# Kernel tuning notes

Measured on AMD Instinct MI355X. Metric: run time of the kernel, lower is better.

## Reference

```python
import jax, jax.numpy as jnp
import numpy as np

N = 50000      # nodes
E = 640000     # edges
FIN = 100      # raw node feature dim (nn.Linear(100, d_model))
D = 128        # d_model (dim_hidden)
H = 8          # num_heads
DH = D // H    # head dim
L = 4          # num_layers
DFF = 4 * D    # dim_feedforward
G = 64         # number of graphs in the batch
SCALE = DH ** -0.5


def setup_inputs() -> dict:
    key = jax.random.key(0)
    ks = jax.random.split(key, 12)
    x = jax.random.normal(ks[0], (N, FIN), jnp.float32)
    edge_index = jax.random.randint(ks[1], (2, E), 0, N, dtype=jnp.int64)
    batch = jnp.sort(jax.random.randint(ks[2], (N,), 0, G, dtype=jnp.int64))

    def w(k, shape, fan_in):
        return jax.random.normal(k, shape, jnp.float32) * (fan_in ** -0.5)

    W_embed = w(ks[3], (FIN, D), FIN)          # embedding, bias=False
    Wqk = w(ks[4], (L, D, 2 * D), D)           # to_qk, bias=False
    Wv = w(ks[5], (L, D, D), D)                # to_v, bias=False
    Wout = w(ks[6], (L, D, D), D)              # out_proj
    b_out = jnp.zeros((L, D), jnp.float32)
    W1 = w(ks[7], (L, D, DFF), D)              # FFN linear1
    b1 = jnp.zeros((L, DFF), jnp.float32)
    W2 = w(ks[8], (L, DFF, D), DFF)            # FFN linear2
    b2 = jnp.zeros((L, D), jnp.float32)
    return dict(x=x, edge_index=edge_index, batch=batch, W_embed=W_embed,
                Wqk=Wqk, Wv=Wv, Wout=Wout, b_out=b_out, W1=W1, b1=b1,
                W2=W2, b2=b2)


def reference(x, edge_index, batch, W_embed, Wqk, Wv, Wout, b_out, W1, b1, W2, b2):
    src = edge_index[0]  # j (message source)
    dst = edge_index[1]  # i (aggregation target)
    h = x @ W_embed  # [N, D]; dropout is identity at eval
    for l in range(L):
        # --- DAG multi-head attention (PyG MessagePassing, aggr='add') ---
        qk = h @ Wqk[l]
        q, k = qk[:, :D], qk[:, D:]
        v = h @ Wv[l]
        qj = q[src].reshape(E, H, DH)   # qk_j: gathered at source
        ki = k[dst].reshape(E, H, DH)   # qk_i: gathered at target
        logits = (qj * ki).sum(-1) * SCALE  # [E, H]
        # segment softmax over edges sharing the same target node
        m = jax.ops.segment_max(logits, dst, num_segments=N)        # [N, H]
        p = jnp.exp(logits - m[dst])
        ssum = jax.ops.segment_sum(p, dst, num_segments=N)          # [N, H]
        attn = p / ssum[dst]
        msg = (v[src].reshape(E, H, DH) * attn[:, :, None]).reshape(E, D)
        agg = jax.ops.segment_sum(msg, dst, num_segments=N)         # [N, D]
        h = h + (agg @ Wout[l] + b_out[l])   # residual; norm1 = Identity
        # --- FFN (relu) ---
        ff = jax.nn.relu(h @ W1[l] + b1[l]) @ W2[l] + b2[l]
        h = h + ff                            # residual; norm2 = Identity
    # global mean pool over graphs
    cnt = jax.ops.segment_sum(jnp.ones((N,), h.dtype), batch, num_segments=G)
    pooled = jax.ops.segment_sum(h, batch, num_segments=G) / jnp.maximum(cnt, 1.0)[:, None]
    return pooled
```

## Files before the change

kernel.cpp:

```cpp
#include <hip/hip_runtime.h>
#include <hip/hip_bf16.h>
#include <math.h>

#define D 128
#define NH 8
#define DFF 512
#define NG 64
#define NL 4
#define FIN 100
#define SCALE 0.25f
#define QKV 384

typedef __attribute__((ext_vector_type(8))) short short8;
typedef __attribute__((ext_vector_type(4))) float f32x4;

__device__ inline unsigned short f2bf(float v) {
    __hip_bfloat16 b = __float2bfloat16(v);
    return *reinterpret_cast<unsigned short*>(&b);
}

__global__ void count_kernel(const int* __restrict__ dst, int* __restrict__ cnt, int E) {
    int e = blockIdx.x * 256 + threadIdx.x;
    if (e < E) atomicAdd(&cnt[dst[e]], 1);
}

__global__ __launch_bounds__(1024) void scan_block_kernel(const int* __restrict__ cnt,
        int* __restrict__ incl, int* __restrict__ partials, int n) {
    __shared__ int s[1024];
    int tid = threadIdx.x;
    int gid = blockIdx.x * 1024 + tid;
    int val = (gid < n) ? cnt[gid] : 0;
    s[tid] = val;
    __syncthreads();
    for (int o = 1; o < 1024; o <<= 1) {
        int t = (tid >= o) ? s[tid - o] : 0;
        __syncthreads();
        s[tid] += t;
        __syncthreads();
    }
    if (gid < n) incl[gid] = s[tid];
    if (tid == 1023) partials[blockIdx.x] = s[1023];
}

__global__ void scan_partials_kernel(int* __restrict__ partials, int nb) {
    if (threadIdx.x == 0 && blockIdx.x == 0) {
        int run = 0;
        for (int i = 0; i < nb; ++i) { int t = partials[i]; partials[i] = run; run += t; }
    }
}

__global__ void finalize_off_kernel(const int* __restrict__ cnt, const int* __restrict__ incl,
        const int* __restrict__ partials, int* __restrict__ off, int* __restrict__ cur,
        int n, int E) {
    int gid = blockIdx.x * 256 + threadIdx.x;
    if (gid < n) {
        int v = incl[gid] - cnt[gid] + partials[gid >> 10];
        off[gid] = v;
        cur[gid] = v;
    }
    if (gid == 0) off[n] = E;
}

__global__ void scatter_kernel(const int* __restrict__ src, const int* __restrict__ dst,
        int* __restrict__ cur, int* __restrict__ csr_src, int E) {
    int e = blockIdx.x * 256 + threadIdx.x;
    if (e < E) {
        int p = atomicAdd(&cur[dst[e]], 1);
        csr_src[p] = src[e];
    }
}

__global__ void transpose_cvt_kernel(const float* __restrict__ W, __hip_bfloat16* __restrict__ Bt,
        int K, int N, int ldl) {
    int l = blockIdx.y;
    const float* w = W + (size_t)l * K * N;
    __hip_bfloat16* bt = Bt + (size_t)l * ldl;
    int idx = blockIdx.x * 256 + threadIdx.x;
    if (idx >= K * N) return;
    int n = idx / K, k = idx - n * K;
    bt[(size_t)n * K + k] = __float2bfloat16(w[(size_t)k * N + n]);
}

__global__ void pad_cvt_x_kernel(const float* __restrict__ x, __hip_bfloat16* __restrict__ xb, int n) {
    int idx = blockIdx.x * 256 + threadIdx.x;
    if (idx >= n * 128) return;
    int r = idx >> 7, c = idx & 127;
    xb[idx] = (c < FIN) ? __float2bfloat16(x[(size_t)r * FIN + c]) : __float2bfloat16(0.f);
}

__global__ void wembT_kernel(const float* __restrict__ W, __hip_bfloat16* __restrict__ Bt) {
    int idx = blockIdx.x * 256 + threadIdx.x;
    if (idx >= 128 * 128) return;
    int n = idx >> 7, k = idx & 127;
    Bt[idx] = (k < FIN) ? __float2bfloat16(W[(size_t)k * 128 + n]) : __float2bfloat16(0.f);
}

template<int EPI>
__global__ __launch_bounds__(256) void gemm_mfma(
        const __hip_bfloat16* __restrict__ A, const __hip_bfloat16* __restrict__ Bt,
        const float* __restrict__ bias,
        float* __restrict__ Cf, __hip_bfloat16* __restrict__ Cb,
        int M, int N, int K) {
    __shared__ __align__(16) unsigned short As[128][64];
    __shared__ __align__(16) unsigned short Bs[64][64];
    int t = threadIdx.x;
    int wave = t >> 6, lane = t & 63;
    int row0 = blockIdx.x * 128, col0 = blockIdx.y * 64;
    f32x4 acc[2][4] = {};

    int sr = t >> 3;
    int sc = t & 7;

    for (int k0 = 0; k0 < K; k0 += 64) {
#pragma unroll
        for (int i = 0; i < 4; ++i) {
            int r = i * 32 + sr;
            int gr = row0 + r;
            if (gr >= M) gr = M - 1;
            *reinterpret_cast<short8*>(&As[r][(sc ^ (r & 7)) << 3]) =
                *reinterpret_cast<const short8*>(&A[(size_t)gr * K + k0 + (sc << 3)]);
        }
#pragma unroll
        for (int i = 0; i < 2; ++i) {
            int r = i * 32 + sr;
            *reinterpret_cast<short8*>(&Bs[r][(sc ^ (r & 7)) << 3]) =
                *reinterpret_cast<const short8*>(&Bt[(size_t)(col0 + r) * K + k0 + (sc << 3)]);
        }
        __syncthreads();
#pragma unroll
        for (int kk = 0; kk < 64; kk += 32) {
            int lr = lane & 15;
            int kc = (kk >> 3) + (lane >> 4);
            short8 a[2], b[4];
#pragma unroll
            for (int m = 0; m < 2; ++m) {
                int r = wave * 32 + m * 16 + lr;
                a[m] = *reinterpret_cast<const short8*>(&As[r][(kc ^ (r & 7)) << 3]);
            }
#pragma unroll
            for (int n = 0; n < 4; ++n) {
                int r = n * 16 + lr;
                b[n] = *reinterpret_cast<const short8*>(&Bs[r][(kc ^ (r & 7)) << 3]);
            }
#pragma unroll
            for (int m = 0; m < 2; ++m)
#pragma unroll
                for (int n = 0; n < 4; ++n)
                    acc[m][n] = __builtin_amdgcn_mfma_f32_16x16x32_bf16(a[m], b[n], acc[m][n], 0, 0, 0);
        }
        __syncthreads();
    }

    int lr = lane & 15, rg = (lane >> 4) * 4;
#pragma unroll
    for (int m = 0; m < 2; ++m) {
#pragma unroll
        for (int n = 0; n < 4; ++n) {
            int col = col0 + n * 16 + lr;
#pragma unroll
            for (int j = 0; j < 4; ++j) {
                int row = row0 + wave * 32 + m * 16 + rg + j;
                if (row < M) {
                    float val = acc[m][n][j];
                    if (EPI == 0) {
                        Cb[(size_t)row * N + col] = __float2bfloat16(val);
                    } else {
                        Cf[(size_t)row * N + col] = val;
                        Cb[(size_t)row * N + col] = __float2bfloat16(val);
                    }
                }
            }
        }
    }
}

__global__ __launch_bounds__(256) void fused_out_ffn(
        const __hip_bfloat16* __restrict__ aggb, const __hip_bfloat16* __restrict__ WoutT,
        const float* __restrict__ b_out,
        const __hip_bfloat16* __restrict__ W1T, const float* __restrict__ b1,
        const __hip_bfloat16* __restrict__ W2T, const float* __restrict__ b2,
        float* __restrict__ h32, __hip_bfloat16* __restrict__ hb, int M) {
    extern __shared__ __align__(16) unsigned short smem[];
    unsigned short* As  = smem;
    unsigned short* Bs  = smem + 16384;
    unsigned short* W1s = Bs;
    unsigned short* ff1s = Bs + 8192;
    unsigned short* W2s = smem + 32768;

    int t = threadIdx.x;
    int wave = t >> 6, lane = t & 63;
    int lr = lane & 15, lg = lane >> 4;
    int row0 = blockIdx.x * 128;

#pragma unroll
    for (int i = 0; i < 8; ++i) {
        int idx = t + i * 256;
        int r = idx >> 4, ch = idx & 15;
        int gr = row0 + r; if (gr >= M) gr = M - 1;
        *reinterpret_cast<short8*>(&As[r * 128 + ((ch ^ (r & 7)) << 3)]) =
            *reinterpret_cast<const short8*>(&aggb[(size_t)gr * 128 + ch * 8]);
        *reinterpret_cast<short8*>(&Bs[r * 128 + ((ch ^ (r & 7)) << 3)]) =
            *reinterpret_cast<const short8*>(&WoutT[(size_t)r * 128 + ch * 8]);
    }
    __syncthreads();

    f32x4 acc1[2][8] = {};
#pragma unroll
    for (int kk4 = 0; kk4 < 4; ++kk4) {
        int kc = kk4 * 4 + lg;
        short8 a[2], b[8];
#pragma unroll
        for (int m = 0; m < 2; ++m) {
            int r = wave * 32 + m * 16 + lr;
            a[m] = *reinterpret_cast<const short8*>(&As[r * 128 + ((kc ^ (r & 7)) << 3)]);
        }
#pragma unroll
        for (int n = 0; n < 8; ++n) {
            int r = n * 16 + lr;
            b[n] = *reinterpret_cast<const short8*>(&Bs[r * 128 + ((kc ^ (r & 7)) << 3)]);
        }
#pragma unroll
        for (int m = 0; m < 2; ++m)
#pragma unroll
            for (int n = 0; n < 8; ++n)
                acc1[m][n] = __builtin_amdgcn_mfma_f32_16x16x32_bf16(a[m], b[n], acc1[m][n], 0, 0, 0);
    }

#pragma unroll
    for (int m = 0; m < 2; ++m) {
#pragma unroll
        for (int n = 0; n < 8; ++n) {
            int col = n * 16 + lr;
            float bo = b_out[col];
#pragma unroll
            for (int j = 0; j < 4; ++j) {
                int rl = wave * 32 + m * 16 + lg * 4 + j;
                int row = row0 + rl;
                float hv = (row < M) ? h32[(size_t)row * 128 + col] : 0.f;
                float val = acc1[m][n][j] + bo + hv;
                if (row < M) h32[(size_t)row * 128 + col] = val;
                As[rl * 128 + (((col >> 3) ^ (rl & 7)) << 3) + (col & 7)] = f2bf(val);
            }
        }
    }

    f32x4 h2acc[2][8] = {};
    for (int c = 0; c < 8; ++c) {
        __syncthreads();
#pragma unroll
        for (int i = 0; i < 4; ++i) {
            int idx = t + i * 256;
            int r = idx >> 4, ch = idx & 15;
            *reinterpret_cast<short8*>(&W1s[r * 128 + ((ch ^ (r & 7)) << 3)]) =
                *reinterpret_cast<const short8*>(&W1T[((size_t)(c * 64 + r)) * 128 + ch * 8]);
        }
#pragma unroll
        for (int i = 0; i < 4; ++i) {
            int idx = t + i * 256;
            int r = idx >> 3, ch = idx & 7;
            *reinterpret_cast<short8*>(&W2s[r * 64 + ((ch ^ (r & 7)) << 3)]) =
                *reinterpret_cast<const short8*>(&W2T[(size_t)r * 512 + c * 64 + ch * 8]);
        }
        __syncthreads();
        f32x4 acc2[2][4] = {};
#pragma unroll
        for (int kk4 = 0; kk4 < 4; ++kk4) {
            int kc = kk4 * 4 + lg;
            short8 a[2], b[4];
#pragma unroll
            for (int m = 0; m < 2; ++m) {
                int r = wave * 32 + m * 16 + lr;
                a[m] = *reinterpret_cast<const short8*>(&As[r * 128 + ((kc ^ (r & 7)) << 3)]);
            }
#pragma unroll
            for (int n = 0; n < 4; ++n) {
                int r = n * 16 + lr;
                b[n] = *reinterpret_cast<const short8*>(&W1s[r * 128 + ((kc ^ (r & 7)) << 3)]);
            }
#pragma unroll
            for (int m = 0; m < 2; ++m)
#pragma unroll
                for (int n = 0; n < 4; ++n)
                    acc2[m][n] = __builtin_amdgcn_mfma_f32_16x16x32_bf16(a[m], b[n], acc2[m][n], 0, 0, 0);
        }
#pragma unroll
        for (int m = 0; m < 2; ++m) {
#pragma unroll
            for (int n = 0; n < 4; ++n) {
                int col = n * 16 + lr;
                float bb = b1[c * 64 + col];
#pragma unroll
                for (int j = 0; j < 4; ++j) {
                    int rl = wave * 32 + m * 16 + lg * 4 + j;
                    float val = fmaxf(acc2[m][n][j] + bb, 0.f);
                    ff1s[rl * 64 + (((col >> 3) ^ (rl & 7)) << 3) + (col & 7)] = f2bf(val);
                }
            }
        }
#pragma unroll
        for (int kk4 = 0; kk4 < 2; ++kk4) {
            int kc = kk4 * 4 + lg;
            short8 a[2], b[8];
#pragma unroll
            for (int m = 0; m < 2; ++m) {
                int r = wave * 32 + m * 16 + lr;
                a[m] = *reinterpret_cast<const short8*>(&ff1s[r * 64 + ((kc ^ (r & 7)) << 3)]);
            }
#pragma unroll
            for (int n = 0; n < 8; ++n) {
                int r = n * 16 + lr;
                b[n] = *reinterpret_cast<const short8*>(&W2s[r * 64 + ((kc ^ (r & 7)) << 3)]);
            }
#pragma unroll
            for (int m = 0; m < 2; ++m)
#pragma unroll
                for (int n = 0; n < 8; ++n)
                    h2acc[m][n] = __builtin_amdgcn_mfma_f32_16x16x32_bf16(a[m], b[n], h2acc[m][n], 0, 0, 0);
        }
    }

#pragma unroll
    for (int m = 0; m < 2; ++m) {
#pragma unroll
        for (int n = 0; n < 8; ++n) {
            int col = n * 16 + lr;
            float bb = b2[col];
#pragma unroll
            for (int j = 0; j < 4; ++j) {
                int row = row0 + wave * 32 + m * 16 + lg * 4 + j;
                if (row < M) {
                    float val = h2acc[m][n][j] + bb + h32[(size_t)row * 128 + col];
                    h32[(size_t)row * 128 + col] = val;
                    hb[(size_t)row * 128 + col] = __float2bfloat16(val);
                }
            }
        }
    }
}

__global__ __launch_bounds__(256) void attn_kernel(const __hip_bfloat16* __restrict__ qkvb,
        const int* __restrict__ off, const int* __restrict__ csr_src,
        __hip_bfloat16* __restrict__ aggb, int n) {
    int wave = threadIdx.x >> 6;
    int lane = threadIdx.x & 63;
    int i = blockIdx.x * 4 + wave;
    if (i >= n) return;
    const unsigned* qv = reinterpret_cast<const unsigned*>(qkvb);
    unsigned ku = qv[(size_t)i * 192 + 64 + lane];
    float kx = __uint_as_float(ku << 16);
    float ky = __uint_as_float(ku & 0xffff0000u);
    int e0 = off[i], e1 = off[i + 1];
    float m = -INFINITY, ssum = 0.f, ax = 0.f, ay = 0.f;
    int e = e0;
    for (; e + 4 <= e1; e += 4) {
        int s0 = csr_src[e], s1 = csr_src[e + 1], s2 = csr_src[e + 2], s3 = csr_src[e + 3];
        unsigned q0 = qv[(size_t)s0 * 192 + lane];
        unsigned q1 = qv[(size_t)s1 * 192 + lane];
        unsigned q2 = qv[(size_t)s2 * 192 + lane];
        unsigned q3 = qv[(size_t)s3 * 192 + lane];
        unsigned w0 = qv[(size_t)s0 * 192 + 128 + lane];
        unsigned w1 = qv[(size_t)s1 * 192 + 128 + lane];
        unsigned w2 = qv[(size_t)s2 * 192 + 128 + lane];
        unsigned w3 = qv[(size_t)s3 * 192 + 128 + lane];
        float l0 = __uint_as_float(q0 << 16) * kx + __uint_as_float(q0 & 0xffff0000u) * ky;
        float l1 = __uint_as_float(q1 << 16) * kx + __uint_as_float(q1 & 0xffff0000u) * ky;
        float l2 = __uint_as_float(q2 << 16) * kx + __uint_as_float(q2 & 0xffff0000u) * ky;
        float l3 = __uint_as_float(q3 << 16) * kx + __uint_as_float(q3 & 0xffff0000u) * ky;
        l0 += __shfl_xor(l0, 1); l1 += __shfl_xor(l1, 1); l2 += __shfl_xor(l2, 1); l3 += __shfl_xor(l3, 1);
        l0 += __shfl_xor(l0, 2); l1 += __shfl_xor(l1, 2); l2 += __shfl_xor(l2, 2); l3 += __shfl_xor(l3, 2);
        l0 += __shfl_xor(l0, 4); l1 += __shfl_xor(l1, 4); l2 += __shfl_xor(l2, 4); l3 += __shfl_xor(l3, 4);
        l0 *= SCALE; l1 *= SCALE; l2 *= SCALE; l3 *= SCALE;
        float mx = fmaxf(fmaxf(l0, l1), fmaxf(l2, l3));
        float mn = fmaxf(m, mx);
        float corr = __expf(m - mn);
        float p0 = __expf(l0 - mn);
        float p1 = __expf(l1 - mn);
        float p2 = __expf(l2 - mn);
        float p3 = __expf(l3 - mn);
        ssum = ssum * corr + ((p0 + p1) + (p2 + p3));
        ax = ax * corr + p0 * __uint_as_float(w0 << 16) + p1 * __uint_as_float(w1 << 16)
                       + p2 * __uint_as_float(w2 << 16) + p3 * __uint_as_float(w3 << 16);
        ay = ay * corr + p0 * __uint_as_float(w0 & 0xffff0000u) + p1 * __uint_as_float(w1 & 0xffff0000u)
                       + p2 * __uint_as_float(w2 & 0xffff0000u) + p3 * __uint_as_float(w3 & 0xffff0000u);
        m = mn;
    }
    for (; e < e1; ++e) {
        int s0 = csr_src[e];
        unsigned q0 = qv[(size_t)s0 * 192 + lane];
        unsigned w0 = qv[(size_t)s0 * 192 + 128 + lane];
        float l0 = __uint_as_float(q0 << 16) * kx + __uint_as_float(q0 & 0xffff0000u) * ky;
        l0 += __shfl_xor(l0, 1); l0 += __shfl_xor(l0, 2); l0 += __shfl_xor(l0, 4);
        l0 *= SCALE;
        float mn = fmaxf(m, l0);
        float corr = __expf(m - mn);
        float pe = __expf(l0 - mn);
        ssum = ssum * corr + pe;
        ax = ax * corr + pe * __uint_as_float(w0 << 16);
        ay = ay * corr + pe * __uint_as_float(w0 & 0xffff0000u);
        m = mn;
    }
    float inv = (ssum > 0.f) ? 1.f / ssum : 0.f;
    __hip_bfloat162 o;
    o.x = __float2bfloat16(ax * inv);
    o.y = __float2bfloat16(ay * inv);
    *reinterpret_cast<__hip_bfloat162*>(aggb + (size_t)i * 128 + lane * 2) = o;
}

__global__ void group_bounds_kernel(const int* __restrict__ batch, int n, int* __restrict__ gstart) {
    int g = threadIdx.x;
    if (g > NG) return;
    int lo = 0, hi = n;
    while (lo < hi) {
        int mid = (lo + hi) >> 1;
        if (batch[mid] < g) lo = mid + 1; else hi = mid;
    }
    gstart[g] = lo;
}

__global__ __launch_bounds__(256) void pool_stage1(const float* __restrict__ h,
        const int* __restrict__ gstart, float* __restrict__ pws) {
    int g = blockIdx.x, sub = blockIdx.y;
    int s = gstart[g], e = gstart[g + 1];
    int c = threadIdx.x & 127;
    int half = threadIdx.x >> 7;
    float acc = 0.f;
    for (int r = s + sub * 2 + half; r < e; r += 16)
        acc += h[(size_t)r * 128 + c];
    __shared__ float tmp[2][128];
    tmp[half][c] = acc;
    __syncthreads();
    if (half == 0)
        pws[((size_t)g * 8 + sub) * 128 + c] = tmp[0][c] + tmp[1][c];
}

__global__ void pool_stage2(const float* __restrict__ pws, const int* __restrict__ gstart,
        float* __restrict__ out) {
    int g = blockIdx.x, c = threadIdx.x;
    float s = 0.f;
#pragma unroll
    for (int i = 0; i < 8; ++i) s += pws[((size_t)g * 8 + i) * 128 + c];
    float cntf = (float)(gstart[g + 1] - gstart[g]);
    out[(size_t)g * 128 + c] = s / fmaxf(cntf, 1.f);
}

extern "C" void kernel_launch(void* const* d_in, const int* in_sizes, int n_in,
                              void* d_out, int out_size, void* d_ws, size_t ws_size,
                              hipStream_t stream) {
    const float* x = (const float*)d_in[0];
    const int* ei = (const int*)d_in[1];
    const int* batch = (const int*)d_in[2];
    const float* W_embed = (const float*)d_in[3];
    const float* Wqk = (const float*)d_in[4];
    const float* Wv = (const float*)d_in[5];
    const float* Wout = (const float*)d_in[6];
    const float* b_out = (const float*)d_in[7];
    const float* W1 = (const float*)d_in[8];
    const float* b1 = (const float*)d_in[9];
    const float* W2 = (const float*)d_in[10];
    const float* b2 = (const float*)d_in[11];

    int Nn = in_sizes[2];
    int E = in_sizes[1] / 2;

    char* p = (char*)d_ws;
    auto alloc = [&](size_t bytes) {
        char* r = p;
        p += (bytes + 255) & ~(size_t)255;
        return r;
    };
    float* h32 = (float*)alloc((size_t)Nn * D * 4);
    __hip_bfloat16* hb = (__hip_bfloat16*)alloc((size_t)Nn * D * 2);
    __hip_bfloat16* aggb = (__hip_bfloat16*)alloc((size_t)Nn * D * 2);
    __hip_bfloat16* qkvb = (__hip_bfloat16*)alloc((size_t)Nn * QKV * 2);
    __hip_bfloat16* xb = (__hip_bfloat16*)alloc((size_t)Nn * D * 2);
    __hip_bfloat16* WembT = (__hip_bfloat16*)alloc((size_t)D * D * 2);
    __hip_bfloat16* WqkvT = (__hip_bfloat16*)alloc((size_t)NL * QKV * D * 2);
    __hip_bfloat16* WoutT = (__hip_bfloat16*)alloc((size_t)NL * D * D * 2);
    __hip_bfloat16* W1T = (__hip_bfloat16*)alloc((size_t)NL * D * DFF * 2);
    __hip_bfloat16* W2T = (__hip_bfloat16*)alloc((size_t)NL * DFF * D * 2);
    int* csr_src = (int*)alloc((size_t)E * 4);
    int* cnt = (int*)alloc((size_t)Nn * 4);
    int* incl = (int*)alloc((size_t)Nn * 4);
    int* off = (int*)alloc(((size_t)Nn + 1) * 4);
    int* cur = (int*)alloc((size_t)Nn * 4);
    int* partials = (int*)alloc(1024 * 4);
    int* gstart = (int*)alloc((NG + 1) * 4);
    float* pws = (float*)alloc((size_t)NG * 8 * 128 * 4);

    const int* e_src = ei;
    const int* e_dst = ei + E;

    hipMemsetAsync(cnt, 0, (size_t)Nn * 4, stream);
    count_kernel<<<(E + 255) / 256, 256, 0, stream>>>(e_dst, cnt, E);
    int nsb = (Nn + 1023) / 1024;
    scan_block_kernel<<<nsb, 1024, 0, stream>>>(cnt, incl, partials, Nn);
    scan_partials_kernel<<<1, 64, 0, stream>>>(partials, nsb);
    finalize_off_kernel<<<(Nn + 255) / 256, 256, 0, stream>>>(cnt, incl, partials, off, cur, Nn, E);
    scatter_kernel<<<(E + 255) / 256, 256, 0, stream>>>(e_src, e_dst, cur, csr_src, E);

    transpose_cvt_kernel<<<dim3((2 * D * D + 255) / 256, NL), 256, 0, stream>>>(
        Wqk, WqkvT, D, 2 * D, QKV * D);
    transpose_cvt_kernel<<<dim3((D * D + 255) / 256, NL), 256, 0, stream>>>(
        Wv, WqkvT + (size_t)2 * D * D, D, D, QKV * D);
    transpose_cvt_kernel<<<dim3((D * D + 255) / 256, NL), 256, 0, stream>>>(
        Wout, WoutT, D, D, D * D);
    transpose_cvt_kernel<<<dim3((D * DFF + 255) / 256, NL), 256, 0, stream>>>(
        W1, W1T, D, DFF, D * DFF);
    transpose_cvt_kernel<<<dim3((DFF * D + 255) / 256, NL), 256, 0, stream>>>(
        W2, W2T, DFF, D, DFF * D);
    wembT_kernel<<<(128 * 128 + 255) / 256, 256, 0, stream>>>(W_embed, WembT);
    pad_cvt_x_kernel<<<((size_t)Nn * 128 + 255) / 256, 256, 0, stream>>>(x, xb, Nn);

    int gmb = (Nn + 127) / 128;
    gemm_mfma<3><<<dim3(gmb, D / 64), 256, 0, stream>>>(
        xb, WembT, nullptr, h32, hb, Nn, D, D);

    size_t fused_lds = (size_t)(16384 + 16384 + 8192) * sizeof(unsigned short);

    for (int l = 0; l < NL; ++l) {
        gemm_mfma<0><<<dim3(gmb, QKV / 64), 256, 0, stream>>>(
            hb, WqkvT + (size_t)l * QKV * D, nullptr, nullptr, qkvb, Nn, QKV, D);
        attn_kernel<<<(Nn + 3) / 4, 256, 0, stream>>>(qkvb, off, csr_src, aggb, Nn);
        fused_out_ffn<<<gmb, 256, fused_lds, stream>>>(
            aggb, WoutT + (size_t)l * D * D, b_out + (size_t)l * D,
            W1T + (size_t)l * D * DFF, b1 + (size_t)l * DFF,
            W2T + (size_t)l * DFF * D, b2 + (size_t)l * D,
            h32, hb, Nn);
    }

    group_bounds_kernel<<<1, 128, 0, stream>>>(batch, Nn, gstart);
    pool_stage1<<<dim3(NG, 8), 256, 0, stream>>>(h32, gstart, pws);
    pool_stage2<<<NG, 128, 0, stream>>>(pws, gstart, (float*)d_out);
}
```

Before: 664.2 us.

## Add dedicated QKV GEMM and cut LDS and reloads in fused out/FFN kernel

Replaces the generic QKV GEMM (one block per 64-column slice) with a kernel that loads each 128-row A tile once, keeps its fragments in registers, and loops over all six 64-column weight chunks. In the fused out-proj/FFN kernel, the post-attention activations are held in registers instead of being reread from LDS each chunk, and the residual is kept in accumulators so h32 is not reread at the end. LDS is shrunk to 64KB with aliased buffers, and bf16 stores to LDS are packed in pairs via lane shuffles. Launch bounds now request higher occupancy, which adds register pressure and possible spills, and the generic GEMM template drops its EPI branch.

```diff
diff --git a/kernel.cpp b/kernel.cpp
--- a/kernel.cpp
+++ b/kernel.cpp
@@ -162,30 +162,97 @@
                 int row = row0 + wave * 32 + m * 16 + rg + j;
                 if (row < M) {
                     float val = acc[m][n][j];
-                    if (EPI == 0) {
-                        Cb[(size_t)row * N + col] = __float2bfloat16(val);
-                    } else {
-                        Cf[(size_t)row * N + col] = val;
-                        Cb[(size_t)row * N + col] = __float2bfloat16(val);
-                    }
+                    Cf[(size_t)row * N + col] = val;
+                    Cb[(size_t)row * N + col] = __float2bfloat16(val);
                 }
             }
         }
     }
 }
 
-__global__ __launch_bounds__(256) void fused_out_ffn(
+__global__ __launch_bounds__(256, 3) void gemm_qkv(
+        const __hip_bfloat16* __restrict__ A, const __hip_bfloat16* __restrict__ Bt,
+        __hip_bfloat16* __restrict__ Cb, int M) {
+    __shared__ __align__(16) unsigned short As[128 * 128];
+    __shared__ __align__(16) unsigned short Bs[64 * 128];
+    int t = threadIdx.x;
+    int wave = t >> 6, lane = t & 63;
+    int lr = lane & 15, lg = lane >> 4;
+    int row0 = blockIdx.x * 128;
+
+#pragma unroll
+    for (int i = 0; i < 8; ++i) {
+        int idx = t + i * 256;
+        int r = idx >> 4, ch = idx & 15;
+        int gr = row0 + r; if (gr >= M) gr = M - 1;
+        *reinterpret_cast<short8*>(&As[r * 128 + ((ch ^ (r & 7)) << 3)]) =
+            *reinterpret_cast<const short8*>(&A[(size_t)gr * 128 + ch * 8]);
+    }
+
+    short8 a_all[2][4];
+    for (int c = 0; c < 6; ++c) {
+#pragma unroll
+        for (int i = 0; i < 4; ++i) {
+            int idx = t + i * 256;
+            int r = idx >> 4, ch = idx & 15;
+            *reinterpret_cast<short8*>(&Bs[r * 128 + ((ch ^ (r & 7)) << 3)]) =
+                *reinterpret_cast<const short8*>(&Bt[((size_t)(c * 64 + r)) * 128 + ch * 8]);
+        }
+        __syncthreads();
+        if (c == 0) {
+#pragma unroll
+            for (int m = 0; m < 2; ++m)
+#pragma unroll
+                for (int ks = 0; ks < 4; ++ks) {
+                    int r = wave * 32 + m * 16 + lr;
+                    int kc = ks * 4 + lg;
+                    a_all[m][ks] = *reinterpret_cast<const short8*>(&As[r * 128 + ((kc ^ (r & 7)) << 3)]);
+                }
+        }
+        f32x4 acc[2][4] = {};
+#pragma unroll
+        for (int ks = 0; ks < 4; ++ks) {
+            int kc = ks * 4 + lg;
+            short8 b[4];
+#pragma unroll
+            for (int n = 0; n < 4; ++n) {
+                int r = n * 16 + lr;
+                b[n] = *reinterpret_cast<const short8*>(&Bs[r * 128 + ((kc ^ (r & 7)) << 3)]);
+            }
+#pragma unroll
+            for (int m = 0; m < 2; ++m)
+#pragma unroll
+                for (int n = 0; n < 4; ++n)
+                    acc[m][n] = __builtin_amdgcn_mfma_f32_16x16x32_bf16(a_all[m][ks], b[n], acc[m][n], 0, 0, 0);
+        }
+#pragma unroll
+        for (int m = 0; m < 2; ++m)
+#pragma unroll
+            for (int n = 0; n < 4; ++n) {
+                int col = c * 64 + n * 16 + lr;
+#pragma unroll
+                for (int j = 0; j < 4; ++j) {
+                    int row = row0 + wave * 32 + m * 16 + lg * 4 + j;
+                    if (row < M)
+                        Cb[(size_t)row * QKV + col] = __float2bfloat16(acc[m][n][j]);
+                }
+            }
+        __syncthreads();
+    }
+}
+
+__global__ __launch_bounds__(256, 2) void fused_out_ffn(
         const __hip_bfloat16* __restrict__ aggb, const __hip_bfloat16* __restrict__ WoutT,
         const float* __restrict__ b_out,
         const __hip_bfloat16* __restrict__ W1T, const float* __restrict__ b1,
         const __hip_bfloat16* __restrict__ W2T, const float* __restrict__ b2,
         float* __restrict__ h32, __hip_bfloat16* __restrict__ hb, int M) {
-    extern __shared__ __align__(16) unsigned short smem[];
-    unsigned short* As  = smem;
-    unsigned short* Bs  = smem + 16384;
-    unsigned short* W1s = Bs;
-    unsigned short* ff1s = Bs + 8192;
-    unsigned short* W2s = smem + 32768;
+    __shared__ __align__(16) unsigned short smem[32768];
+    unsigned short* As   = smem;
+    unsigned short* Bs   = smem + 16384;
+    unsigned short* W1s  = smem;
+    unsigned short* ff1s = smem + 8192;
+    unsigned short* W2s  = smem + 16384;
 
     int t = threadIdx.x;
     int wave = t >> 6, lane = t & 63;
@@ -206,8 +273,8 @@
 
     f32x4 acc1[2][8] = {};
 #pragma unroll
-    for (int kk4 = 0; kk4 < 4; ++kk4) {
-        int kc = kk4 * 4 + lg;
+    for (int ks = 0; ks < 4; ++ks) {
+        int kc = ks * 4 + lg;
         short8 a[2], b[8];
 #pragma unroll
         for (int m = 0; m < 2; ++m) {
@@ -238,15 +305,31 @@
                 int row = row0 + rl;
                 float hv = (row < M) ? h32[(size_t)row * 128 + col] : 0.f;
                 float val = acc1[m][n][j] + bo + hv;
-                if (row < M) h32[(size_t)row * 128 + col] = val;
-                As[rl * 128 + (((col >> 3) ^ (rl & 7)) << 3) + (col & 7)] = f2bf(val);
-            }
-        }
-    }
+                acc1[m][n][j] = val;
+                float other = __shfl_xor(val, 1);
+                if (!(lane & 1)) {
+                    unsigned lo16 = f2bf(val), hi16 = f2bf(other);
+                    int ch = col >> 3;
+                    int addr = rl * 128 + ((ch ^ (rl & 7)) << 3) + (col & 7);
+                    *reinterpret_cast<unsigned*>(&As[addr]) = lo16 | (hi16 << 16);
+                }
+            }
+        }
+    }
+
+    short8 a_ff[2][4];
+#pragma unroll
+    for (int m = 0; m < 2; ++m)
+#pragma unroll
+        for (int ks = 0; ks < 4; ++ks) {
+            int r = wave * 32 + m * 16 + lr;
+            int kc = ks * 4 + lg;
+            a_ff[m][ks] = *reinterpret_cast<const short8*>(&As[r * 128 + ((kc ^ (r & 7)) << 3)]);
+        }
+    __syncthreads();
 
     f32x4 h2acc[2][8] = {};
     for (int c = 0; c < 8; ++c) {
-        __syncthreads();
 #pragma unroll
         for (int i = 0; i < 4; ++i) {
             int idx = t + i * 256;
@@ -262,16 +345,12 @@
                 *reinterpret_cast<const short8*>(&W2T[(size_t)r * 512 + c * 64 + ch * 8]);
         }
         __syncthreads();
+
         f32x4 acc2[2][4] = {};
 #pragma unroll
-        for (int kk4 = 0; kk4 < 4; ++kk4) {
-            int kc = kk4 * 4 + lg;
-            short8 a[2], b[4];
-#pragma unroll
-            for (int m = 0; m < 2; ++m) {
-                int r = wave * 32 + m * 16 + lr;
-                a[m] = *reinterpret_cast<const short8*>(&As[r * 128 + ((kc ^ (r & 7)) << 3)]);
-            }
+        for (int ks = 0; ks < 4; ++ks) {
+            int kc = ks * 4 + lg;
+            short8 b[4];
 #pragma unroll
             for (int n = 0; n < 4; ++n) {
                 int r = n * 16 + lr;
@@ -281,7 +360,7 @@
             for (int m = 0; m < 2; ++m)
 #pragma unroll
                 for (int n = 0; n < 4; ++n)
-                    acc2[m][n] = __builtin_amdgcn_mfma_f32_16x16x32_bf16(a[m], b[n], acc2[m][n], 0, 0, 0);
+                    acc2[m][n] = __builtin_amdgcn_mfma_f32_16x16x32_bf16(a_ff[m][ks], b[n], acc2[m][n], 0, 0, 0);
         }
 #pragma unroll
         for (int m = 0; m < 2; ++m) {
@@ -293,18 +372,24 @@
                 for (int j = 0; j < 4; ++j) {
                     int rl = wave * 32 + m * 16 + lg * 4 + j;
                     float val = fmaxf(acc2[m][n][j] + bb, 0.f);
-                    ff1s[rl * 64 + (((col >> 3) ^ (rl & 7)) << 3) + (col & 7)] = f2bf(val);
+                    float other = __shfl_xor(val, 1);
+                    if (!(lane & 1)) {
+                        unsigned lo16 = f2bf(val), hi16 = f2bf(other);
+                        int ch = col >> 3;
+                        int addr = rl * 64 + ((ch ^ (rl & 7)) << 3) + (col & 7);
+                        *reinterpret_cast<unsigned*>(&ff1s[addr]) = lo16 | (hi16 << 16);
+                    }
                 }
             }
         }
 #pragma unroll
-        for (int kk4 = 0; kk4 < 2; ++kk4) {
-            int kc = kk4 * 4 + lg;
-            short8 a[2], b[8];
+        for (int ks = 0; ks < 2; ++ks) {
+            int kc = ks * 4 + lg;
+            short8 a2[2], b[8];
 #pragma unroll
             for (int m = 0; m < 2; ++m) {
                 int r = wave * 32 + m * 16 + lr;
-                a[m] = *reinterpret_cast<const short8*>(&ff1s[r * 64 + ((kc ^ (r & 7)) << 3)]);
+                a2[m] = *reinterpret_cast<const short8*>(&ff1s[r * 64 + ((kc ^ (r & 7)) << 3)]);
             }
 #pragma unroll
             for (int n = 0; n < 8; ++n) {
@@ -315,8 +400,9 @@
             for (int m = 0; m < 2; ++m)
 #pragma unroll
                 for (int n = 0; n < 8; ++n)
-                    h2acc[m][n] = __builtin_amdgcn_mfma_f32_16x16x32_bf16(a[m], b[n], h2acc[m][n], 0, 0, 0);
-        }
+                    h2acc[m][n] = __builtin_amdgcn_mfma_f32_16x16x32_bf16(a2[m], b[n], h2acc[m][n], 0, 0, 0);
+        }
+        __syncthreads();
     }
 
 #pragma unroll
@@ -329,7 +415,7 @@
             for (int j = 0; j < 4; ++j) {
                 int row = row0 + wave * 32 + m * 16 + lg * 4 + j;
                 if (row < M) {
-                    float val = h2acc[m][n][j] + bb + h32[(size_t)row * 128 + col];
+                    float val = acc1[m][n][j] + h2acc[m][n][j] + bb;
                     h32[(size_t)row * 128 + col] = val;
                     hb[(size_t)row * 128 + col] = __float2bfloat16(val);
                 }
@@ -515,13 +601,10 @@
     gemm_mfma<3><<<dim3(gmb, D / 64), 256, 0, stream>>>(
         xb, WembT, nullptr, h32, hb, Nn, D, D);
 
-    size_t fused_lds = (size_t)(16384 + 16384 + 8192) * sizeof(unsigned short);
-
     for (int l = 0; l < NL; ++l) {
-        gemm_mfma<0><<<dim3(gmb, QKV / 64), 256, 0, stream>>>(
-            hb, WqkvT + (size_t)l * QKV * D, nullptr, nullptr, qkvb, Nn, QKV, D);
+        gemm_qkv<<<gmb, 256, 0, stream>>>(hb, WqkvT + (size_t)l * QKV * D, qkvb, Nn);
         attn_kernel<<<(Nn + 3) / 4, 256, 0, stream>>>(qkvb, off, csr_src, aggb, Nn);
-        fused_out_ffn<<<gmb, 256, fused_lds, stream>>>(
+        fused_out_ffn<<<gmb, 256, 0, stream>>>(
             aggb, WoutT + (size_t)l * D * D, b_out + (size_t)l * D,
             W1T + (size_t)l * D * DFF, b1 + (size_t)l * DFF,
             W2T + (size_t)l * DFF * D, b2 + (size_t)l * D,
```

Measured after the change: 700.4 us. 1.05x slower.
